# Kernel optimization log

Hardware: AMD Instinct MI355X
Metric: run time of the kernel (lower is better)

The kernel has to match this reference:

```python
import jax, jax.numpy as jnp
import numpy as np

B, L, D_MODEL, H, MAX_DIST = 4, 1024, 1024, 16, 64
DEPTH = D_MODEL // H
VOCAB = 2 * MAX_DIST + 1


def setup_inputs() -> dict:
    key = jax.random.key(0)
    ks = jax.random.split(key, 12)
    s = 0.02
    return {
        "x": jax.random.normal(ks[0], (B, L, D_MODEL), jnp.float32),
        "mask": jnp.zeros((B, 1, 1, L), jnp.float32),
        "wq": jax.random.normal(ks[1], (D_MODEL, D_MODEL), jnp.float32) * s,
        "bq": jnp.zeros((D_MODEL,), jnp.float32),
        "wk": jax.random.normal(ks[2], (D_MODEL, D_MODEL), jnp.float32) * s,
        "bk": jnp.zeros((D_MODEL,), jnp.float32),
        "wv": jax.random.normal(ks[3], (D_MODEL, D_MODEL), jnp.float32) * s,
        "bv": jnp.zeros((D_MODEL,), jnp.float32),
        "wo": jax.random.normal(ks[4], (D_MODEL, D_MODEL), jnp.float32) * s,
        "bo": jnp.zeros((D_MODEL,), jnp.float32),
        "rel_k_table": jax.random.normal(ks[5], (VOCAB, DEPTH), jnp.float32) * s,
        "rel_v_table": jax.random.normal(ks[6], (VOCAB, DEPTH), jnp.float32) * s,
    }


def _split_heads(t):
    # [B, L, d_model] -> [B, H, L, depth]
    return t.reshape(B, L, H, DEPTH).transpose(0, 2, 1, 3)


def reference(x, mask, wq, bq, wk, bk, wv, bv, wo, bo, rel_k_table, rel_v_table):
    # q/k/v projections (self-attention)
    q = _split_heads(x @ wq + bq)
    k = _split_heads(x @ wk + bk)
    v = _split_heads(x @ wv + bv)

    # relative positions matrix [L, L], clipped to [-MAX_DIST, MAX_DIST] then shifted
    r = jnp.arange(L)
    rel_mat = jnp.clip(r[None, :] - r[:, None], -MAX_DIST, MAX_DIST) + MAX_DIST
    rel_k = rel_k_table[rel_mat]  # [L, L, depth]
    rel_v = rel_v_table[rel_mat]  # [L, L, depth]

    # _relative_attention_inner(q, k, rel_k, transpose=True):
    # logits = q k^T + q . rel_k  (note: t2t relative path applies no 1/sqrt(dk) scale)
    logits = (jnp.einsum('bhqd,bhkd->bhqk', q, k)
              + jnp.einsum('bhqd,qkd->bhqk', q, rel_k))
    logits = logits + mask * (-1e9)  # bias
    weights = jax.nn.softmax(logits, axis=-1)  # [B, H, L, L]

    # _relative_attention_inner(weights, v, rel_v, transpose=False)
    ctx = (jnp.einsum('bhqk,bhkd->bhqd', weights, v)
           + jnp.einsum('bhqk,qkd->bhqd', weights, rel_v))

    # combine heads and output projection
    ctx = ctx.transpose(0, 2, 1, 3).reshape(B, L, D_MODEL)
    out = ctx @ wo + bo
    return out
```

## Files before the change

### kernel.cpp

```cpp
#include <hip/hip_runtime.h>
#include <hip/hip_bf16.h>
#include <cstdint>
#include <cstddef>

typedef unsigned int u32;
typedef __attribute__((ext_vector_type(8))) short s16x8;
typedef __attribute__((ext_vector_type(4))) short s16x4;
typedef __attribute__((ext_vector_type(4))) float f32x4;
typedef __attribute__((ext_vector_type(2))) u32   u32x2;

#define MFMA(a,b,c) __builtin_amdgcn_mfma_f32_16x16x32_bf16(a,b,c,0,0,0)

#if __has_builtin(__builtin_amdgcn_mfma_f32_16x16x16bf16_1k)
#define MFMA16(a,b,c) __builtin_amdgcn_mfma_f32_16x16x16bf16_1k(a,b,c,0,0,0)
#else
static __device__ __forceinline__ f32x4 MFMA16(s16x4 a, s16x4 b, f32x4 c){
    f32x4 d;
    asm("v_mfma_f32_16x16x16_bf16 %0, %1, %2, %3"
        : "=v"(d) : "v"(a), "v"(b), "v"(c));
    return d;
}
#endif

#define LOG2E 1.4426950408889634f

__device__ __forceinline__ float fexp2(float x) {
    return __builtin_amdgcn_exp2f(x);
}

__device__ __forceinline__ short f2bf(float f) {
    u32 u = __builtin_bit_cast(u32, f);
    u32 r = (u + 0x7fffu + ((u >> 16) & 1u)) >> 16;
    return (short)r;
}
__device__ __forceinline__ float bf2f(short s) {
    return __builtin_bit_cast(float, ((u32)(unsigned short)s) << 16);
}
__device__ __forceinline__ u32 cvtpk(float lo, float hi) {
    u32 r;
    asm("v_cvt_pk_bf16_f32 %0, %1, %2" : "=v"(r) : "v"(lo), "v"(hi));
    return r;
}
__device__ __forceinline__ void async_copy16(void* lds, const void* g) {
    __builtin_amdgcn_global_load_lds((const __attribute__((address_space(1))) u32*)g,
                                     (__attribute__((address_space(3))) u32*)lds, 16, 0, 0);
}

__global__ __launch_bounds__(256)
void prep_all(const float* __restrict__ x, short* __restrict__ xb,
              const float* __restrict__ wq, const float* __restrict__ wk,
              const float* __restrict__ wv, const float* __restrict__ wo,
              short* __restrict__ Wtqkv, short* __restrict__ Wto,
              const float* __restrict__ relk, const float* __restrict__ relv,
              short* __restrict__ relkb, short* __restrict__ relvT,
              const float* __restrict__ mask, short* __restrict__ maskPb)
{
    __shared__ float sT[64][68];
    const int bid = blockIdx.x;
    const int tid = threadIdx.x;

    if (bid < 2048) {
        int i = (bid * 256 + tid) * 8;
        float4 a = *(const float4*)&x[i];
        float4 b = *(const float4*)&x[i + 4];
        s16x8 v = { f2bf(a.x), f2bf(a.y), f2bf(a.z), f2bf(a.w),
                    f2bf(b.x), f2bf(b.y), f2bf(b.z), f2bf(b.w) };
        *(s16x8*)&xb[i] = v;
    } else if (bid < 3072) {
        const int wid = bid - 2048;
        const int kt = wid & 15, nt = (wid >> 4) & 15, seg = wid >> 8;
        const float* src = seg == 0 ? wq : seg == 1 ? wk : seg == 2 ? wv : wo;
        const int k0 = kt * 64, n0 = nt * 64;
#pragma unroll
        for (int i = 0; i < 4; ++i) {
            int t2 = tid + i * 256;
            int r = t2 >> 4, c4 = t2 & 15;
            *(float4*)&sT[r][c4 * 4] = *(const float4*)&src[(size_t)(k0 + r) * 1024 + n0 + c4 * 4];
        }
        __syncthreads();
#pragma unroll
        for (int i = 0; i < 2; ++i) {
            int t2 = tid + i * 256;
            int rn = t2 >> 3, ch = t2 & 7;
            s16x8 v;
#pragma unroll
            for (int j = 0; j < 8; ++j) v[j] = f2bf(sT[ch * 8 + j][rn]);
            if (seg < 3)
                *(s16x8*)&Wtqkv[(size_t)(seg * 1024 + n0 + rn) * 1024 + k0 + ch * 8] = v;
            else
                *(s16x8*)&Wto[(size_t)(n0 + rn) * 1024 + k0 + ch * 8] = v;
        }
    } else {
        int gt = (bid - 3072) * 256 + tid;
        for (int i = gt; i < 144 * 64; i += 256 * 8) {
            int r = i >> 6, d = i & 63;
            relkb[i] = (r < 129) ? f2bf(relk[r * 64 + d]) : (short)0;
        }
        for (int i = gt; i < 64 * 128; i += 256 * 8) {
            int d = i >> 7, r = i & 127;
            relvT[i] = f2bf(relv[r * 64 + d]);
        }
        for (int i = gt; i < 4096; i += 256 * 8)
            maskPb[i] = f2bf(mask[i] * (-1e9f * LOG2E));
    }
}

__global__ __launch_bounds__(256, 4)
void gemm_qkv(const short* __restrict__ Ab, const short* __restrict__ Wt,
              const float* __restrict__ bq, const float* __restrict__ bk,
              const float* __restrict__ bv,
              short* __restrict__ Qb, short* __restrict__ Kb, short* __restrict__ Vtb)
{
    __shared__ __align__(16) short As[128 * 64];
    __shared__ __align__(16) short Bs[128 * 64];
    const int tid = threadIdx.x;
    const int w = tid >> 6, lane = tid & 63;
    const int lo16 = lane & 15, hi = lane >> 4;
    const int pb = blockIdx.x;
    const int wg = (pb & 7) * 96 + (pb >> 3);
    const int n0g = (wg % 24) * 128;
    const int m0 = (wg / 24) * 128;
    const int wr = w >> 1, wc = w & 1;

    f32x4 acc[4][4] = {};

    for (int t = 0; t < 16; ++t) {
        const int k0 = t * 64;
        __syncthreads();
#pragma unroll
        for (int i = 0; i < 4; ++i) {
            int o = i * 4096 + tid * 16;
            int row = o >> 7;
            int cb = o & 127;
            int sc = cb ^ ((row & 7) << 4);
            async_copy16((char*)As + o, Ab + (size_t)(m0 + row) * 1024 + k0 + (sc >> 1));
            async_copy16((char*)Bs + o, Wt + (size_t)(n0g + row) * 1024 + k0 + (sc >> 1));
        }
        __syncthreads();
#pragma unroll
        for (int ks = 0; ks < 2; ++ks) {
            s16x8 aF[4], bF[4];
#pragma unroll
            for (int mi = 0; mi < 4; ++mi) {
                int row = wr * 64 + mi * 16 + lo16;
                int cb = ks * 64 + hi * 16;
                aF[mi] = *(const s16x8*)((const char*)As + row * 128 + (cb ^ ((row & 7) << 4)));
            }
#pragma unroll
            for (int ni = 0; ni < 4; ++ni) {
                int row = wc * 64 + ni * 16 + lo16;
                int cb = ks * 64 + hi * 16;
                bF[ni] = *(const s16x8*)((const char*)Bs + row * 128 + (cb ^ ((row & 7) << 4)));
            }
#pragma unroll
            for (int mi = 0; mi < 4; ++mi)
#pragma unroll
                for (int ni = 0; ni < 4; ++ni)
                    acc[mi][ni] = MFMA(aF[mi], bF[ni], acc[mi][ni]);
        }
    }

    const int seg = n0g >> 10;
    const int nn = n0g & 1023;
    const float* bias = seg == 0 ? bq : seg == 1 ? bk : bv;
    const float oscale = (seg == 0) ? LOG2E : 1.0f;
    float bv4[4];
#pragma unroll
    for (int ni = 0; ni < 4; ++ni) bv4[ni] = bias[nn + wc * 64 + ni * 16 + lo16];

    if (seg == 2) {
#pragma unroll
        for (int mi = 0; mi < 4; ++mi)
#pragma unroll
            for (int ni = 0; ni < 4; ++ni) {
                int nl = nn + wc * 64 + ni * 16 + lo16;
                int hh = nl >> 6, d = nl & 63;
                int mbase = m0 + wr * 64 + mi * 16 + hi * 4;
                int bb = mbase >> 10, l0 = mbase & 1023;
                int j0 = l0 & 31;
                int col = (l0 >> 5) * 32 + (((j0 >> 4) & 1) << 2) + (((j0 >> 2) & 3) << 3);
                s16x4 pk = { f2bf(acc[mi][ni][0] + bv4[ni]),
                             f2bf(acc[mi][ni][1] + bv4[ni]),
                             f2bf(acc[mi][ni][2] + bv4[ni]),
                             f2bf(acc[mi][ni][3] + bv4[ni]) };
                *(s16x4*)&Vtb[((size_t)(bb * 16 + hh) * 64 + d) * 1024 + col] = pk;
            }
    } else {
        short* out = seg == 0 ? Qb : Kb;
#pragma unroll
        for (int mi = 0; mi < 4; ++mi)
#pragma unroll
            for (int ni = 0; ni < 4; ++ni) {
                int nl = nn + wc * 64 + ni * 16 + lo16;
                int hh = nl >> 6, d = nl & 63;
#pragma unroll
                for (int r = 0; r < 4; ++r) {
                    int m = m0 + wr * 64 + mi * 16 + hi * 4 + r;
                    int bb = m >> 10, l = m & 1023;
                    out[(((size_t)bb * 16 + hh) * 1024 + l) * 64 + d] =
                        f2bf((acc[mi][ni][r] + bv4[ni]) * oscale);
                }
            }
    }
}

__global__ __launch_bounds__(256, 4)
void attn_mfma(const short* __restrict__ Qb, const short* __restrict__ Kb,
               const short* __restrict__ Vtb, const short* __restrict__ relkb,
               const short* __restrict__ relvTb, const float* __restrict__ relv_f32,
               const short* __restrict__ maskPb, short* __restrict__ CTXb)
{
    __shared__ __align__(16) short sK[2][32 * 64];
    __shared__ __align__(16) short sV[2][64 * 32];
    __shared__ __align__(16) short sQB[4][16][128];

    const int tid = threadIdx.x;
    const int w = tid >> 6, lane = tid & 63;
    const int lo16 = lane & 15, hi = lane >> 4;
    const int qsw = (lo16 & 7) << 4;
    const int vm = (lo16 >> 1) & 3;

    const int p = blockIdx.x;
    const int bid = (p & 7) * 128 + (p >> 3);
    const int bh = bid >> 4;
    const int qt = bid & 15;
    const int b = bh >> 4, h = bh & 15;
    const int q0 = qt * 64 + w * 16;
    const int q_abs = q0 + lo16;

    const short* Kbase = Kb + (size_t)bh * 65536;
    const short* Vtbase = Vtb + (size_t)bh * 65536;
    const short* mbase = maskPb + b * 1024;

    const int skr = tid >> 3, skc = tid & 7;
    const int svd = tid >> 2, svc = tid & 3;
    const short* ksrc = Kbase + (size_t)skr * 64 + ((skc ^ (skr & 7)) << 3);
    const short* vsrc = Vtbase + (size_t)svd * 1024 + ((svc ^ ((svd >> 1) & 3)) << 3);

    async_copy16((char*)&sK[0][0] + tid * 16, ksrc);
    async_copy16((char*)&sV[0][0] + tid * 16, vsrc);

    const short* qptr = Qb + ((size_t)bh * 1024 + q_abs) * 64 + hi * 8;
    const s16x8 qB0 = *(const s16x8*)qptr;
    const s16x8 qB1 = *(const s16x8*)(qptr + 32);

    f32x4 dq8 = {0.f, 0.f, 0.f, 0.f};
#pragma unroll
    for (int rf = 0; rf < 9; ++rf) {
        const short* rp = relkb + (size_t)(rf * 16 + lo16) * 64 + hi * 8;
        s16x8 rA0 = *(const s16x8*)rp;
        s16x8 rA1 = *(const s16x8*)(rp + 32);
        f32x4 dq = {0.f, 0.f, 0.f, 0.f};
        dq = MFMA(rA0, qB0, dq);
        dq = MFMA(rA1, qB1, dq);
        if (rf < 8) {
            s16x4 pk = { f2bf(dq[0]), f2bf(dq[1]), f2bf(dq[2]), f2bf(dq[3]) };
            *(s16x4*)&sQB[w][lo16][(rf * 16 + hi * 4) ^ qsw] = pk;
        } else {
            dq8 = dq;
        }
    }
    const float qrel_lo = bf2f(sQB[w][lo16][0 ^ qsw]);
    const float qrel_hi = __shfl(bf2f(f2bf(dq8[0])), lo16);

    __syncthreads();

    f32x4 ctx[4] = {};
    float lsum = 0.f, lov = 0.f, hiv = 0.f;
    const f32x4 z = {0.f, 0.f, 0.f, 0.f};
    const int km = lo16 & 7;

    for (int t = 0; t < 32; ++t) {
        const int kf = t * 32;
        const int cur = t & 1, nxt = (t + 1) & 1;
        const int kfn = ((t + 1) & 31) * 32;
        async_copy16((char*)&sK[nxt][0] + tid * 16, ksrc + (size_t)kfn * 64);
        async_copy16((char*)&sV[nxt][0] + tid * 16, vsrc + kfn);
        s16x8 kr0 = *(const s16x8*)(sK[cur] + lo16 * 64 + ((hi ^ km) << 3));
        s16x8 kr1 = *(const s16x8*)(sK[cur] + lo16 * 64 + (((hi + 4) ^ km) << 3));
        s16x8 kr2 = *(const s16x8*)(sK[cur] + (lo16 + 16) * 64 + ((hi ^ km) << 3));
        s16x8 kr3 = *(const s16x8*)(sK[cur] + (lo16 + 16) * 64 + (((hi + 4) ^ km) << 3));
        s16x8 vr0 = *(const s16x8*)(sV[cur] + lo16 * 32 + ((hi ^ vm) << 3));
        s16x8 vr1 = *(const s16x8*)(sV[cur] + (16 + lo16) * 32 + ((hi ^ vm) << 3));
        s16x8 vr2 = *(const s16x8*)(sV[cur] + (32 + lo16) * 32 + ((hi ^ vm) << 3));
        s16x8 vr3 = *(const s16x8*)(sV[cur] + (48 + lo16) * 32 + ((hi ^ vm) << 3));
        s16x4 m0 = *(const s16x4*)&mbase[kf + hi * 4];
        s16x4 m1 = *(const s16x4*)&mbase[kf + 16 + hi * 4];

        __builtin_amdgcn_s_setprio(1);
        f32x4 s0 = MFMA(kr0, qB0, z);
        f32x4 s1 = MFMA(kr2, qB0, z);
        s0 = MFMA(kr1, qB1, s0);
        s1 = MFMA(kr3, qB1, s1);
        __builtin_amdgcn_s_setprio(0);

        float pr[8];
        if (kf + 95 <= q0 || kf >= q0 + 79) {
            const float qc = (kf < q0) ? qrel_lo : qrel_hi;
            float bs = 0.f;
#pragma unroll
            for (int r = 0; r < 4; ++r) {
                pr[r]     = fexp2(s0[r] + qc + bf2f(m0[r]));
                pr[4 + r] = fexp2(s1[r] + qc + bf2f(m1[r]));
            }
#pragma unroll
            for (int r = 0; r < 8; ++r) bs += pr[r];
            lsum += bs;
            if (kf < q0) lov += bs; else hiv += bs;
        } else {
#pragma unroll
            for (int f = 0; f < 2; ++f)
#pragma unroll
                for (int r = 0; r < 4; ++r) {
                    int k_abs = kf + f * 16 + hi * 4 + r;
                    int dd = k_abs - q_abs;
                    dd = dd < -64 ? -64 : (dd > 64 ? 64 : dd);
                    int rel = dd + 64;
                    int relc = rel > 127 ? 127 : rel;
                    float qv = bf2f(sQB[w][lo16][relc ^ qsw]);
                    if (rel == 128) qv = qrel_hi;
                    float sv = f ? s1[r] : s0[r];
                    float mv = bf2f(f ? m1[r] : m0[r]);
                    float pex = fexp2(sv + qv + mv);
                    pr[f * 4 + r] = pex;
                    lsum += pex;
                    if (rel >= 1 && rel <= 127) sQB[w][lo16][rel ^ qsw] = f2bf(pex);
                    else if (rel == 0) lov += pex;
                    else hiv += pex;
                }
        }
        u32x2 w0 = { cvtpk(pr[0], pr[1]), cvtpk(pr[2], pr[3]) };
        u32x2 w1 = { cvtpk(pr[4], pr[5]), cvtpk(pr[6], pr[7]) };
        s16x4 pf0 = __builtin_bit_cast(s16x4, w0);
        s16x4 pf1 = __builtin_bit_cast(s16x4, w1);

        s16x4 a0 = __builtin_shufflevector(vr0, vr0, 0, 1, 2, 3);
        s16x4 b0 = __builtin_shufflevector(vr0, vr0, 4, 5, 6, 7);
        s16x4 a1 = __builtin_shufflevector(vr1, vr1, 0, 1, 2, 3);
        s16x4 b1 = __builtin_shufflevector(vr1, vr1, 4, 5, 6, 7);
        s16x4 a2 = __builtin_shufflevector(vr2, vr2, 0, 1, 2, 3);
        s16x4 b2 = __builtin_shufflevector(vr2, vr2, 4, 5, 6, 7);
        s16x4 a3 = __builtin_shufflevector(vr3, vr3, 0, 1, 2, 3);
        s16x4 b3 = __builtin_shufflevector(vr3, vr3, 4, 5, 6, 7);
        __builtin_amdgcn_s_setprio(1);
        ctx[0] = MFMA16(a0, pf0, ctx[0]);
        ctx[1] = MFMA16(a1, pf0, ctx[1]);
        ctx[2] = MFMA16(a2, pf0, ctx[2]);
        ctx[3] = MFMA16(a3, pf0, ctx[3]);
        ctx[0] = MFMA16(b0, pf1, ctx[0]);
        ctx[1] = MFMA16(b1, pf1, ctx[1]);
        ctx[2] = MFMA16(b2, pf1, ctx[2]);
        ctx[3] = MFMA16(b3, pf1, ctx[3]);
        __builtin_amdgcn_s_setprio(0);

        __syncthreads();
    }

    if (hi == 0) {
        sQB[w][lo16][0 ^ qsw] = 0;
        if (qt == 0) {
            for (int rel = 1; rel <= 63 - q_abs; ++rel)
                sQB[w][lo16][rel ^ qsw] = 0;
        } else if (qt == 15) {
            for (int rel = 1088 - q_abs; rel <= 127; ++rel)
                sQB[w][lo16][rel ^ qsw] = 0;
        }
    }
    __syncthreads();

#pragma unroll
    for (int ks = 0; ks < 4; ++ks) {
        s16x8 bB = *(const s16x8*)&sQB[w][lo16][(ks * 32 + hi * 8) ^ qsw];
#pragma unroll
        for (int df = 0; df < 4; ++df) {
            s16x8 rA = *(const s16x8*)(relvTb + (size_t)(df * 16 + lo16) * 128 + ks * 32 + hi * 8);
            ctx[df] = MFMA(rA, bB, ctx[df]);
        }
    }

    lsum += __shfl_xor(lsum, 16); lsum += __shfl_xor(lsum, 32);
    lov  += __shfl_xor(lov, 16);  lov  += __shfl_xor(lov, 32);
    hiv  += __shfl_xor(hiv, 16);  hiv  += __shfl_xor(hiv, 32);
    const float inv = 1.0f / lsum;

#pragma unroll
    for (int df = 0; df < 4; ++df) {
        s16x4 pk;
#pragma unroll
        for (int r = 0; r < 4; ++r) {
            int d = df * 16 + hi * 4 + r;
            float t = ctx[df][r] + lov * relv_f32[d] + hiv * relv_f32[128 * 64 + d];
            pk[r] = f2bf(t * inv);
        }
        *(s16x4*)(CTXb + ((size_t)(b * 1024) + q_abs) * 1024 + h * 64 + df * 16 + hi * 4) = pk;
    }
}

__global__ __launch_bounds__(256, 4)
void gemm_out(const short* __restrict__ Ab, const short* __restrict__ Wto,
              const float* __restrict__ bo, float* __restrict__ out)
{
    __shared__ __align__(16) short As[128 * 64];
    __shared__ __align__(16) short Bs[64 * 64];
    const int tid = threadIdx.x;
    const int w = tid >> 6, lane = tid & 63;
    const int lo16 = lane & 15, hi = lane >> 4;
    const int pb = blockIdx.x;
    const int wg = (pb & 7) * 64 + (pb >> 3);
    const int n0 = (wg & 15) * 64;
    const int m0 = (wg >> 4) * 128;
    const int wr = w;

    f32x4 acc[2][4] = {};

    for (int t = 0; t < 16; ++t) {
        const int k0 = t * 64;
        __syncthreads();
#pragma unroll
        for (int i = 0; i < 4; ++i) {
            int o = i * 4096 + tid * 16;
            int row = o >> 7;
            int cb = o & 127;
            int sc = cb ^ ((row & 7) << 4);
            async_copy16((char*)As + o, Ab + (size_t)(m0 + row) * 1024 + k0 + (sc >> 1));
        }
#pragma unroll
        for (int i = 0; i < 2; ++i) {
            int o = i * 4096 + tid * 16;
            int row = o >> 7;
            int cb = o & 127;
            int sc = cb ^ ((row & 7) << 4);
            async_copy16((char*)Bs + o, Wto + (size_t)(n0 + row) * 1024 + k0 + (sc >> 1));
        }
        __syncthreads();
#pragma unroll
        for (int ks = 0; ks < 2; ++ks) {
            s16x8 aF[2], bF[4];
#pragma unroll
            for (int mi = 0; mi < 2; ++mi) {
                int row = wr * 32 + mi * 16 + lo16;
                int cb = ks * 64 + hi * 16;
                aF[mi] = *(const s16x8*)((const char*)As + row * 128 + (cb ^ ((row & 7) << 4)));
            }
#pragma unroll
            for (int ni = 0; ni < 4; ++ni) {
                int row = ni * 16 + lo16;
                int cb = ks * 64 + hi * 16;
                bF[ni] = *(const s16x8*)((const char*)Bs + row * 128 + (cb ^ ((row & 7) << 4)));
            }
#pragma unroll
            for (int mi = 0; mi < 2; ++mi)
#pragma unroll
                for (int ni = 0; ni < 4; ++ni)
                    acc[mi][ni] = MFMA(aF[mi], bF[ni], acc[mi][ni]);
        }
    }

    float bv4[4];
#pragma unroll
    for (int ni = 0; ni < 4; ++ni) bv4[ni] = bo[n0 + ni * 16 + lo16];
#pragma unroll
    for (int mi = 0; mi < 2; ++mi)
#pragma unroll
        for (int ni = 0; ni < 4; ++ni)
#pragma unroll
            for (int r = 0; r < 4; ++r) {
                int m = m0 + wr * 32 + mi * 16 + hi * 4 + r;
                out[(size_t)m * 1024 + n0 + ni * 16 + lo16] = acc[mi][ni][r] + bv4[ni];
            }
}

extern "C" void kernel_launch(void* const* d_in, const int* in_sizes, int n_in,
                              void* d_out, int out_size, void* d_ws, size_t ws_size,
                              hipStream_t stream)
{
    (void)in_sizes; (void)n_in; (void)out_size; (void)ws_size;
    const float* x    = (const float*)d_in[0];
    const float* mask = (const float*)d_in[1];
    const float* wq   = (const float*)d_in[2];
    const float* bq   = (const float*)d_in[3];
    const float* wk   = (const float*)d_in[4];
    const float* bk   = (const float*)d_in[5];
    const float* wv   = (const float*)d_in[6];
    const float* bv   = (const float*)d_in[7];
    const float* wo   = (const float*)d_in[8];
    const float* bo   = (const float*)d_in[9];
    const float* relk = (const float*)d_in[10];
    const float* relv = (const float*)d_in[11];
    float* out = (float*)d_out;

    char* p = (char*)d_ws;
    short* xb     = (short*)p; p += (size_t)4096 * 1024 * 2;
    short* Wtqkv  = (short*)p; p += (size_t)3072 * 1024 * 2;
    short* Wto    = (short*)p; p += (size_t)1024 * 1024 * 2;
    short* Qb     = (short*)p; p += (size_t)4096 * 1024 * 2;
    short* Kb     = (short*)p; p += (size_t)4096 * 1024 * 2;
    short* Vtb    = (short*)p; p += (size_t)4096 * 1024 * 2;
    short* CTXb   = (short*)p; p += (size_t)4096 * 1024 * 2;
    short* relkb  = (short*)p; p += (size_t)144 * 64 * 2;
    short* relvT  = (short*)p; p += (size_t)64 * 128 * 2;
    short* maskPb = (short*)p; p += (size_t)4096 * 2;

    prep_all  <<<3080, 256, 0, stream>>>(x, xb, wq, wk, wv, wo, Wtqkv, Wto,
                                         relk, relv, relkb, relvT, mask, maskPb);
    gemm_qkv  <<<768, 256, 0, stream>>>(xb, Wtqkv, bq, bk, bv, Qb, Kb, Vtb);
    attn_mfma <<<1024, 256, 0, stream>>>(Qb, Kb, Vtb, relkb, relvT, relv, maskPb, CTXb);
    gemm_out  <<<512, 256, 0, stream>>>(CTXb, Wto, bo, out);
}
```

Before: 115.0 us.

## Software-pipeline QK^T scores one tile ahead with triple-buffered K/V shared memory

Moves the K/V shared-memory staging from double to triple buffering, with two tiles prefetched before the loop. The QK^T MFMAs for tile t+1 now run while tile t's scores go through exp and the PV MFMAs, using rotating buffer pointers. The goal is to overlap matrix-core work with the exp/VALU softmax work and hide LDS load latency. In exchange it uses more LDS and holds an extra score tile in registers, which could reduce occupancy under the 256x4 launch bound.

```diff
diff --git a/kernel.cpp b/kernel.cpp
--- a/kernel.cpp
+++ b/kernel.cpp
@@ -210,8 +210,8 @@
                const short* __restrict__ relvTb, const float* __restrict__ relv_f32,
                const short* __restrict__ maskPb, short* __restrict__ CTXb)
 {
-    __shared__ __align__(16) short sK[2][32 * 64];
-    __shared__ __align__(16) short sV[2][64 * 32];
+    __shared__ __align__(16) short sK[3][32 * 64];
+    __shared__ __align__(16) short sV[3][64 * 32];
     __shared__ __align__(16) short sQB[4][16][128];
 
     const int tid = threadIdx.x;
@@ -239,6 +239,8 @@
 
     async_copy16((char*)&sK[0][0] + tid * 16, ksrc);
     async_copy16((char*)&sV[0][0] + tid * 16, vsrc);
+    async_copy16((char*)&sK[1][0] + tid * 16, ksrc + (size_t)32 * 64);
+    async_copy16((char*)&sV[1][0] + tid * 16, vsrc + 32);
 
     const short* qptr = Qb + ((size_t)bh * 1024 + q_abs) * 64 + hi * 8;
     const s16x8 qB0 = *(const s16x8*)qptr;
@@ -270,28 +272,41 @@
     const f32x4 z = {0.f, 0.f, 0.f, 0.f};
     const int km = lo16 & 7;
 
+    const short* sKc = sK[0]; const short* sKn = sK[1]; const short* sKs = sK[2];
+    const short* sVc = sV[0]; const short* sVn = sV[1]; const short* sVs = sV[2];
+
+    f32x4 cS0, cS1;
+    {
+        s16x8 kr0 = *(const s16x8*)(sKc + lo16 * 64 + ((hi ^ km) << 3));
+        s16x8 kr1 = *(const s16x8*)(sKc + lo16 * 64 + (((hi + 4) ^ km) << 3));
+        s16x8 kr2 = *(const s16x8*)(sKc + (lo16 + 16) * 64 + ((hi ^ km) << 3));
+        s16x8 kr3 = *(const s16x8*)(sKc + (lo16 + 16) * 64 + (((hi + 4) ^ km) << 3));
+        cS0 = MFMA(kr0, qB0, z);
+        cS1 = MFMA(kr2, qB0, z);
+        cS0 = MFMA(kr1, qB1, cS0);
+        cS1 = MFMA(kr3, qB1, cS1);
+    }
+
     for (int t = 0; t < 32; ++t) {
         const int kf = t * 32;
-        const int cur = t & 1, nxt = (t + 1) & 1;
-        const int kfn = ((t + 1) & 31) * 32;
-        async_copy16((char*)&sK[nxt][0] + tid * 16, ksrc + (size_t)kfn * 64);
-        async_copy16((char*)&sV[nxt][0] + tid * 16, vsrc + kfn);
-        s16x8 kr0 = *(const s16x8*)(sK[cur] + lo16 * 64 + ((hi ^ km) << 3));
-        s16x8 kr1 = *(const s16x8*)(sK[cur] + lo16 * 64 + (((hi + 4) ^ km) << 3));
-        s16x8 kr2 = *(const s16x8*)(sK[cur] + (lo16 + 16) * 64 + ((hi ^ km) << 3));
-        s16x8 kr3 = *(const s16x8*)(sK[cur] + (lo16 + 16) * 64 + (((hi + 4) ^ km) << 3));
-        s16x8 vr0 = *(const s16x8*)(sV[cur] + lo16 * 32 + ((hi ^ vm) << 3));
-        s16x8 vr1 = *(const s16x8*)(sV[cur] + (16 + lo16) * 32 + ((hi ^ vm) << 3));
-        s16x8 vr2 = *(const s16x8*)(sV[cur] + (32 + lo16) * 32 + ((hi ^ vm) << 3));
-        s16x8 vr3 = *(const s16x8*)(sV[cur] + (48 + lo16) * 32 + ((hi ^ vm) << 3));
+        const int kfn = ((t + 2) & 31) * 32;
+        async_copy16((char*)sKs + tid * 16, ksrc + (size_t)kfn * 64);
+        async_copy16((char*)sVs + tid * 16, vsrc + kfn);
+        s16x8 vr0 = *(const s16x8*)(sVc + lo16 * 32 + ((hi ^ vm) << 3));
+        s16x8 vr1 = *(const s16x8*)(sVc + (16 + lo16) * 32 + ((hi ^ vm) << 3));
+        s16x8 vr2 = *(const s16x8*)(sVc + (32 + lo16) * 32 + ((hi ^ vm) << 3));
+        s16x8 vr3 = *(const s16x8*)(sVc + (48 + lo16) * 32 + ((hi ^ vm) << 3));
         s16x4 m0 = *(const s16x4*)&mbase[kf + hi * 4];
         s16x4 m1 = *(const s16x4*)&mbase[kf + 16 + hi * 4];
-
+        s16x8 kr0 = *(const s16x8*)(sKn + lo16 * 64 + ((hi ^ km) << 3));
+        s16x8 kr1 = *(const s16x8*)(sKn + lo16 * 64 + (((hi + 4) ^ km) << 3));
+        s16x8 kr2 = *(const s16x8*)(sKn + (lo16 + 16) * 64 + ((hi ^ km) << 3));
+        s16x8 kr3 = *(const s16x8*)(sKn + (lo16 + 16) * 64 + (((hi + 4) ^ km) << 3));
         __builtin_amdgcn_s_setprio(1);
-        f32x4 s0 = MFMA(kr0, qB0, z);
-        f32x4 s1 = MFMA(kr2, qB0, z);
-        s0 = MFMA(kr1, qB1, s0);
-        s1 = MFMA(kr3, qB1, s1);
+        f32x4 nS0 = MFMA(kr0, qB0, z);
+        f32x4 nS1 = MFMA(kr2, qB0, z);
+        nS0 = MFMA(kr1, qB1, nS0);
+        nS1 = MFMA(kr3, qB1, nS1);
         __builtin_amdgcn_s_setprio(0);
 
         float pr[8];
@@ -300,8 +315,8 @@
             float bs = 0.f;
 #pragma unroll
             for (int r = 0; r < 4; ++r) {
-                pr[r]     = fexp2(s0[r] + qc + bf2f(m0[r]));
-                pr[4 + r] = fexp2(s1[r] + qc + bf2f(m1[r]));
+                pr[r]     = fexp2(cS0[r] + qc + bf2f(m0[r]));
+                pr[4 + r] = fexp2(cS1[r] + qc + bf2f(m1[r]));
             }
 #pragma unroll
             for (int r = 0; r < 8; ++r) bs += pr[r];
@@ -319,7 +334,7 @@
                     int relc = rel > 127 ? 127 : rel;
                     float qv = bf2f(sQB[w][lo16][relc ^ qsw]);
                     if (rel == 128) qv = qrel_hi;
-                    float sv = f ? s1[r] : s0[r];
+                    float sv = f ? cS1[r] : cS0[r];
                     float mv = bf2f(f ? m1[r] : m0[r]);
                     float pex = fexp2(sv + qv + mv);
                     pr[f * 4 + r] = pex;
@@ -353,6 +368,10 @@
         ctx[3] = MFMA16(b3, pf1, ctx[3]);
         __builtin_amdgcn_s_setprio(0);
 
+        cS0 = nS0; cS1 = nS1;
+        const short* tk = sKc; sKc = sKn; sKn = sKs; sKs = tk;
+        const short* tv = sVc; sVc = sVn; sVn = sVs; sVs = tv;
+
         __syncthreads();
     }
 
```

Result: no change. 113.4 us (-1.3%).
